# Kernel tuning notes

Measured on AMD Instinct MI355X. Metric: run time of the kernel, lower is better.

## Reference

```python
import jax, jax.numpy as jnp
import numpy as np

EMB, HEAD = 2048, 128

def setup_inputs() -> dict:
    key = jax.random.key(0)
    ks = jax.random.split(key, 7)
    x = jax.random.normal(ks[0], (4, 4096, EMB), dtype=jnp.float32)
    s = 1.0 / np.sqrt(EMB)
    wK = jax.random.normal(ks[1], (EMB, HEAD), dtype=jnp.float32) * s
    bK = jax.random.normal(ks[2], (HEAD,), dtype=jnp.float32) * 0.01
    wQ = jax.random.normal(ks[3], (EMB, HEAD), dtype=jnp.float32) * s
    bQ = jax.random.normal(ks[4], (HEAD,), dtype=jnp.float32) * 0.01
    wV = jax.random.normal(ks[5], (EMB, HEAD), dtype=jnp.float32) * s
    bV = jax.random.normal(ks[6], (HEAD,), dtype=jnp.float32) * 0.01
    return {"x": x, "wK": wK, "bK": bK, "wQ": wQ, "bQ": bQ, "wV": wV, "bV": bV}

def reference(x, wK, bK, wQ, bQ, wV, bV):
    B, S, E = x.shape
    K = x @ wK + bK                      # [B,S,H]
    Q = x @ wQ + bQ
    V = x @ wV + bV
    scale = 1.0 / jnp.sqrt(jnp.float32(HEAD))
    att = jnp.einsum('bqh,bkh->bqk', Q, K) * scale   # [B,S,S]
    causal = jnp.tril(jnp.ones((S, S), dtype=bool))
    att = jnp.where(causal, att, -jnp.inf)
    att = jax.nn.softmax(att, axis=-1)
    return jnp.einsum('bqk,bkh->bqh', att, V)        # [B,S,H]
```

## Files before the change

### kernel.cpp

```cpp
#include <hip/hip_runtime.h>
#include <hip/hip_bf16.h>
#include <math.h>

#define SEQ  4096
#define BATCH 4
#define EMBD 2048
#define HDIM 128

#define SCALE_LOG2E 0.12753102721944556f

typedef __bf16 bf16x8 __attribute__((ext_vector_type(8)));
typedef __bf16 bf16x4 __attribute__((ext_vector_type(4)));
typedef float  f32x4  __attribute__((ext_vector_type(4)));

__device__ __forceinline__ bf16x8 ldfrag(const __bf16* p) {
    return *(const bf16x8*)p;
}

__device__ __forceinline__ void gl_lds16(const __bf16* g, __bf16* l) {
    __builtin_amdgcn_global_load_lds(
        (const __attribute__((address_space(1))) void*)g,
        (__attribute__((address_space(3))) void*)l, 16, 0, 0);
}

__global__ __launch_bounds__(256)
void cvt_x(const float* __restrict__ x, __bf16* __restrict__ xb) {
    size_t idx = (size_t)(blockIdx.x * 256 + threadIdx.x) * 8;
    float4 v0 = *(const float4*)(x + idx);
    float4 v1 = *(const float4*)(x + idx + 4);
    bf16x8 o = { (__bf16)v0.x, (__bf16)v0.y, (__bf16)v0.z, (__bf16)v0.w,
                 (__bf16)v1.x, (__bf16)v1.y, (__bf16)v1.z, (__bf16)v1.w };
    *(bf16x8*)(xb + idx) = o;
}

__global__ __launch_bounds__(256)
void cvt_w(const float* __restrict__ wQ, const float* __restrict__ wK,
           const float* __restrict__ wV, __bf16* __restrict__ wt) {
    const float* w = (blockIdx.z == 0) ? wQ : (blockIdx.z == 1) ? wK : wV;
    __bf16* dst = wt + (size_t)blockIdx.z * HDIM * EMBD;
    int k0 = blockIdx.x * 32;
    int n0 = blockIdx.y * 32;
    __shared__ float t[32][33];
    {
        int r  = threadIdx.x >> 3;
        int c4 = (threadIdx.x & 7) * 4;
        float4 v = *(const float4*)(w + (size_t)(k0 + r) * HDIM + n0 + c4);
        t[r][c4 + 0] = v.x; t[r][c4 + 1] = v.y;
        t[r][c4 + 2] = v.z; t[r][c4 + 3] = v.w;
    }
    __syncthreads();
    {
        int n  = threadIdx.x >> 3;
        int k4 = (threadIdx.x & 7) * 4;
        bf16x4 o = { (__bf16)t[k4 + 0][n], (__bf16)t[k4 + 1][n],
                     (__bf16)t[k4 + 2][n], (__bf16)t[k4 + 3][n] };
        *(bf16x4*)(dst + (size_t)(n0 + n) * EMBD + k0 + k4) = o;
    }
}

__global__ __launch_bounds__(256, 3)
void proj(const __bf16* __restrict__ xb,
          const __bf16* __restrict__ wt,
          __bf16* __restrict__ pout) {
    const int mat  = blockIdx.y;
    const int z    = blockIdx.z;
    const int m0   = blockIdx.x * 128;
    const int kb   = z * (EMBD / 2);
    const int wv   = threadIdx.x >> 6;
    const int lane = threadIdx.x & 63;
    const int ln   = lane & 15;
    const int quad = lane >> 4;
    const int r8   = lane >> 3;
    const int c8   = lane & 7;

    __shared__ __bf16 lA[128 * 64];
    __shared__ __bf16 lB[128 * 64];

    const __bf16* wtm = wt + (size_t)mat * (HDIM * EMBD);
    const __bf16* gaS = xb  + (size_t)(m0 + wv * 32 + r8) * EMBD + kb + (c8 ^ r8) * 8;
    const __bf16* gbS = wtm + (size_t)(wv * 32 + r8) * EMBD + kb + (c8 ^ r8) * 8;
    __bf16* laD = lA + (wv * 32) * 64;
    __bf16* lbD = lB + (wv * 32) * 64;

    const int wm0 = (wv >> 1) * 64;
    const int wn0 = (wv & 1) * 64;

    const f32x4 fzero = {0.f, 0.f, 0.f, 0.f};
    f32x4 acc[4][4];
#pragma unroll
    for (int i = 0; i < 4; i++)
#pragma unroll
        for (int j = 0; j < 4; j++) acc[i][j] = fzero;

    for (int k0 = 0; k0 < EMBD / 2; k0 += 64) {
#pragma unroll
        for (int i = 0; i < 4; i++) {
            gl_lds16(gaS + (size_t)i * 8 * EMBD + k0, laD + i * 8 * 64);
            gl_lds16(gbS + (size_t)i * 8 * EMBD + k0, lbD + i * 8 * 64);
        }
        __syncthreads();
#pragma unroll
        for (int kk = 0; kk < 2; kk++) {
            bf16x8 a[4], bb[4];
#pragma unroll
            for (int i = 0; i < 4; i++)
                a[i] = ldfrag(lA + (wm0 + i * 16 + ln) * 64 +
                              (((quad + 4 * kk) ^ (ln & 7)) * 8));
#pragma unroll
            for (int j = 0; j < 4; j++)
                bb[j] = ldfrag(lB + (wn0 + j * 16 + ln) * 64 +
                               (((quad + 4 * kk) ^ (ln & 7)) * 8));
#pragma unroll
            for (int i = 0; i < 4; i++)
#pragma unroll
                for (int j = 0; j < 4; j++)
                    acc[i][j] = __builtin_amdgcn_mfma_f32_16x16x32_bf16(
                        a[i], bb[j], acc[i][j], 0, 0, 0);
        }
        __syncthreads();
    }

    __bf16* pp = pout + (size_t)(mat * 2 + z) * 16384 * 128;
#pragma unroll
    for (int j = 0; j < 4; j++) {
        int col = wn0 + j * 16 + ln;
#pragma unroll
        for (int i = 0; i < 4; i++) {
            int rowb = m0 + wm0 + i * 16 + quad * 4;
#pragma unroll
            for (int r = 0; r < 4; r++)
                pp[(size_t)(rowb + r) * 128 + col] = (__bf16)acc[i][j][r];
        }
    }
}

__global__ __launch_bounds__(256)
void qkv_fin(const __bf16* __restrict__ pout,
             const float* __restrict__ bQ, const float* __restrict__ bK,
             const float* __restrict__ bV,
             __bf16* __restrict__ qws, __bf16* __restrict__ kws,
             __bf16* __restrict__ vtws) {
    const int mat = blockIdx.y;
    const int r0  = blockIdx.x * 16;
    const int t   = threadIdx.x;
    const int rl  = t >> 4;
    const int cc  = (t & 15) * 8;
    const float* bias = (mat == 0) ? bQ : (mat == 1) ? bK : bV;

    bf16x8 p0 = *(const bf16x8*)(pout +
        ((size_t)(mat * 2 + 0) * 16384 + r0 + rl) * 128 + cc);
    bf16x8 p1 = *(const bf16x8*)(pout +
        ((size_t)(mat * 2 + 1) * 16384 + r0 + rl) * 128 + cc);
    float s[8];
#pragma unroll
    for (int i = 0; i < 8; i++)
        s[i] = (float)p0[i] + (float)p1[i] + bias[cc + i];

    if (mat < 2) {
        __bf16* dst = (mat == 0) ? qws : kws;
        bf16x8 o;
#pragma unroll
        for (int i = 0; i < 8; i++) o[i] = (__bf16)s[i];
        *(bf16x8*)(dst + (size_t)(r0 + rl) * 128 + cc) = o;
    } else {
        __shared__ float sm[16][132];
#pragma unroll
        for (int i = 0; i < 8; i++) sm[rl][cc + i] = s[i];
        __syncthreads();
        int col = t >> 1, sg = (t & 1) * 8;
        int bb = r0 >> 12, s0 = r0 & (SEQ - 1);
        bf16x8 o;
#pragma unroll
        for (int i = 0; i < 8; i++) o[i] = (__bf16)sm[sg + i][col];
        *(bf16x8*)(vtws + ((size_t)bb * HDIM + col) * SEQ + s0 + sg) = o;
    }
}

__global__ __launch_bounds__(256, 2)
void attn(const __bf16* __restrict__ qws, const __bf16* __restrict__ kws,
          const __bf16* __restrict__ vtws,
          float* __restrict__ Opart, float* __restrict__ Lpart) {
    const int blk = blockIdx.x;
    const int b   = (blk & 7) >> 1;
    int wi = ((blk >> 3) << 1) | (blk & 1);
    wi = 287 - wi;
    int a = (int)((sqrtf((float)wi + 1.0f) - 1.0f) * 0.5f);
    while (4 * (a + 1) * (a + 2) <= wi) a++;
    while (a > 0 && 4 * a * (a + 1) > wi) a--;
    const int rem = wi - 4 * a * (a + 1);
    const int qt  = a * 8 + rem / (a + 1);
    const int c   = rem - (rem / (a + 1)) * (a + 1);
    const int q0  = qt * 64;
    const int kt0 = c * 8;
    const int kt1 = (kt0 + 8 < qt + 1) ? (kt0 + 8) : (qt + 1);
    const int slot = b * 288 + wi;

    const int wv   = threadIdx.x >> 6;
    const int lane = threadIdx.x & 63;
    const int ln   = lane & 15;
    const int quad = lane >> 4;

    __shared__ __bf16 lK[2][64 * 128];
    __shared__ __bf16 lV[2][128 * 64];
    __shared__ __bf16 lP[4][16 * 72];

    const __bf16* kws_b = kws + (size_t)b * SEQ * HDIM;
    const __bf16* vt_b  = vtws + (size_t)b * HDIM * SEQ;

    const __bf16* qbase =
        qws + ((size_t)(b * SEQ) + q0 + wv * 16 + ln) * HDIM + quad * 8;
    bf16x8 qf[4];
#pragma unroll
    for (int kk = 0; kk < 4; kk++) qf[kk] = ldfrag(qbase + kk * 32);

    const f32x4 fzero = {0.f, 0.f, 0.f, 0.f};
    float lrun[4];
    f32x4 oacc[8];
#pragma unroll
    for (int r = 0; r < 4; r++) lrun[r] = 0.f;
#pragma unroll
    for (int j = 0; j < 8; j++) oacc[j] = fzero;

    const int krow_i = lane >> 4, kslot = lane & 15;
    const int vrow_i = lane >> 3, vslot = lane & 7;

    auto stageK = [&](int k0, int buf) {
#pragma unroll
        for (int i = 0; i < 4; i++) {
            int row = wv * 16 + i * 4 + krow_i;
            const __bf16* src = kws_b + (size_t)(k0 + row) * HDIM +
                                ((kslot ^ (row & 7)) * 8);
            gl_lds16(src, &lK[buf][(wv * 16 + i * 4) * 128]);
        }
    };
    auto stageV = [&](int k0, int buf) {
#pragma unroll
        for (int i = 0; i < 4; i++) {
            int row = wv * 32 + i * 8 + vrow_i;
            const __bf16* src = vt_b + (size_t)row * SEQ + k0 +
                                ((vslot ^ (row & 7)) * 8);
            gl_lds16(src, &lV[buf][(wv * 32 + i * 8) * 64]);
        }
    };

    stageK(kt0 * 64, 0);
    stageV(kt0 * 64, 0);

    for (int kt = kt0; kt < kt1; kt++) {
        __syncthreads();
        const int cur = (kt - kt0) & 1;
        if (kt + 1 < kt1) {
            stageK((kt + 1) * 64, cur ^ 1);
            stageV((kt + 1) * 64, cur ^ 1);
        }

        f32x4 sacc[4];
#pragma unroll
        for (int j = 0; j < 4; j++) sacc[j] = fzero;
        const __bf16* Kb = lK[cur];
#pragma unroll
        for (int j = 0; j < 4; j++) {
#pragma unroll
            for (int kk = 0; kk < 4; kk++) {
                bf16x8 kf = ldfrag(Kb + (j * 16 + ln) * 128 +
                                   (((quad + 4 * kk) ^ (ln & 7)) * 8));
                sacc[j] = __builtin_amdgcn_mfma_f32_16x16x32_bf16(
                    qf[kk], kf, sacc[j], 0, 0, 0);
            }
        }

        const bool diag = (kt == qt);
#pragma unroll
        for (int j = 0; j < 4; j++) {
#pragma unroll
            for (int r = 0; r < 4; r++) {
                float p = exp2f(sacc[j][r] * SCALE_LOG2E);
                if (diag) {
                    int col = kt * 64 + j * 16 + ln;
                    int row = q0 + wv * 16 + quad * 4 + r;
                    if (col > row) p = 0.f;
                }
                lrun[r] += p;
                lP[wv][(quad * 4 + r) * 72 + j * 16 + ln] = (__bf16)p;
            }
        }

        __builtin_amdgcn_s_waitcnt(0xc07f);
        bf16x8 af0 = ldfrag(&lP[wv][ln * 72 + quad * 8]);
        bf16x8 af1 = ldfrag(&lP[wv][ln * 72 + 32 + quad * 8]);

        const __bf16* Vb = lV[cur];
#pragma unroll
        for (int j = 0; j < 8; j++) {
            bf16x8 v0 = ldfrag(Vb + (j * 16 + ln) * 64 +
                               ((quad ^ (ln & 7)) * 8));
            bf16x8 v1 = ldfrag(Vb + (j * 16 + ln) * 64 +
                               (((quad + 4) ^ (ln & 7)) * 8));
            oacc[j] = __builtin_amdgcn_mfma_f32_16x16x32_bf16(
                af0, v0, oacc[j], 0, 0, 0);
            oacc[j] = __builtin_amdgcn_mfma_f32_16x16x32_bf16(
                af1, v1, oacc[j], 0, 0, 0);
        }
    }

#pragma unroll
    for (int r = 0; r < 4; r++) {
#pragma unroll
        for (int off = 8; off >= 1; off >>= 1)
            lrun[r] += __shfl_xor(lrun[r], off);
    }
    if (ln == 0) {
#pragma unroll
        for (int r = 0; r < 4; r++)
            Lpart[(size_t)slot * 64 + wv * 16 + quad * 4 + r] = lrun[r];
    }
    float* Ob = Opart + (size_t)slot * 8192;
#pragma unroll
    for (int r = 0; r < 4; r++) {
        int row = wv * 16 + quad * 4 + r;
#pragma unroll
        for (int j = 0; j < 8; j++)
            Ob[(size_t)row * 128 + j * 16 + ln] = oacc[j][r];
    }
}

__global__ __launch_bounds__(256)
void attn_fin(const float* __restrict__ Opart, const float* __restrict__ Lpart,
              float* __restrict__ out) {
    const int b  = blockIdx.x >> 6;
    const int qt = blockIdx.x & 63;
    const int a  = qt >> 3;
    const int nch = a + 1;
    const int base = b * 288 + 4 * a * (a + 1) + (qt & 7) * (a + 1);
    const int row = threadIdx.x >> 2;
    const int c0  = (threadIdx.x & 3) * 32;

    float l = 0.f;
    f32x4 o[8];
#pragma unroll
    for (int i = 0; i < 8; i++) o[i] = {0.f, 0.f, 0.f, 0.f};
    for (int ch = 0; ch < nch; ch++) {
        const f32x4* Op = (const f32x4*)(Opart + (size_t)(base + ch) * 8192 +
                                         (size_t)row * 128 + c0);
        l += Lpart[(size_t)(base + ch) * 64 + row];
#pragma unroll
        for (int i = 0; i < 8; i++) o[i] += Op[i];
    }
    float inv = 1.f / l;
    f32x4* orow = (f32x4*)(out + ((size_t)(b * SEQ) + qt * 64 + row) * HDIM + c0);
#pragma unroll
    for (int i = 0; i < 8; i++) orow[i] = o[i] * inv;
}

extern "C" void kernel_launch(void* const* d_in, const int* in_sizes, int n_in,
                              void* d_out, int out_size, void* d_ws,
                              size_t ws_size, hipStream_t stream) {
    const float* x  = (const float*)d_in[0];
    const float* wK = (const float*)d_in[1];
    const float* bK = (const float*)d_in[2];
    const float* wQ = (const float*)d_in[3];
    const float* bQ = (const float*)d_in[4];
    const float* wV = (const float*)d_in[5];
    const float* bV = (const float*)d_in[6];
    float* out = (float*)d_out;

    __bf16* xb   = (__bf16*)d_ws;
    __bf16* wt   = xb + (size_t)BATCH * SEQ * EMBD;
    __bf16* qws  = wt + (size_t)3 * HDIM * EMBD;
    __bf16* kws  = qws + (size_t)BATCH * SEQ * HDIM;
    __bf16* vtws = kws + (size_t)BATCH * SEQ * HDIM;
    __bf16* pout = vtws + (size_t)BATCH * SEQ * HDIM;
    float* Opart = (float*)d_ws;
    float* Lpart = Opart + (size_t)1152 * 8192;

    hipLaunchKernelGGL(cvt_w, dim3(EMBD / 32, HDIM / 32, 3), dim3(256), 0,
                       stream, wQ, wK, wV, wt);
    hipLaunchKernelGGL(cvt_x, dim3((size_t)BATCH * SEQ * EMBD / (8 * 256)),
                       dim3(256), 0, stream, x, xb);
    hipLaunchKernelGGL(proj, dim3(SEQ * BATCH / 128, 3, 2), dim3(256), 0,
                       stream, xb, wt, pout);
    hipLaunchKernelGGL(qkv_fin, dim3(SEQ * BATCH / 16, 3), dim3(256), 0,
                       stream, pout, bQ, bK, bV, qws, kws, vtws);
    hipLaunchKernelGGL(attn, dim3(1152), dim3(256), 0, stream,
                       qws, kws, vtws, Opart, Lpart);
    hipLaunchKernelGGL(attn_fin, dim3(256), dim3(256), 0, stream,
                       Opart, Lpart, out);
}
```

Baseline: 312.3 us.

## Fuse QKV projection with bias epilogue, drop split-K and finalize kernel

The projection kernel now computes all three Q/K/V outputs at once for a 64-row tile using 512 threads. It runs over the full K dimension with double-buffered LDS staging, then adds bias and writes Q, K and the transposed V directly through an LDS staging buffer. This removes the split-K partial buffer, its round trip through global memory, and the separate qkv_fin launch. In exchange it uses about 112KB of LDS per block and launches only 256 blocks, which may leave occupancy and load balance weaker than before.

```diff
diff --git a/kernel.cpp b/kernel.cpp
--- a/kernel.cpp
+++ b/kernel.cpp
@@ -58,121 +58,117 @@
     }
 }
 
-__global__ __launch_bounds__(256, 3)
+__global__ __launch_bounds__(512, 2)
 void proj(const __bf16* __restrict__ xb,
           const __bf16* __restrict__ wt,
-          __bf16* __restrict__ pout) {
-    const int mat  = blockIdx.y;
-    const int z    = blockIdx.z;
-    const int m0   = blockIdx.x * 128;
-    const int kb   = z * (EMBD / 2);
-    const int wv   = threadIdx.x >> 6;
+          const float* __restrict__ bQ, const float* __restrict__ bK,
+          const float* __restrict__ bV,
+          __bf16* __restrict__ qws, __bf16* __restrict__ kws,
+          __bf16* __restrict__ vtws) {
+    const int m0   = blockIdx.x * 64;
+    const int w    = threadIdx.x >> 6;
     const int lane = threadIdx.x & 63;
     const int ln   = lane & 15;
     const int quad = lane >> 4;
-    const int r8   = lane >> 3;
-    const int c8   = lane & 7;
-
-    __shared__ __bf16 lA[128 * 64];
-    __shared__ __bf16 lB[128 * 64];
-
-    const __bf16* wtm = wt + (size_t)mat * (HDIM * EMBD);
-    const __bf16* gaS = xb  + (size_t)(m0 + wv * 32 + r8) * EMBD + kb + (c8 ^ r8) * 8;
-    const __bf16* gbS = wtm + (size_t)(wv * 32 + r8) * EMBD + kb + (c8 ^ r8) * 8;
-    __bf16* laD = lA + (wv * 32) * 64;
-    __bf16* lbD = lB + (wv * 32) * 64;
-
-    const int wm0 = (wv >> 1) * 64;
-    const int wn0 = (wv & 1) * 64;
+    const int lr   = lane >> 3;
+    const int lc   = lane & 7;
+
+    __shared__ __bf16 smem[57344];
+
+    const __bf16* gA = xb + (size_t)(m0 + w * 8 + lr) * EMBD + (lc ^ lr) * 8;
+    const __bf16* gB = wt + (size_t)(w * 48 + lr) * EMBD + (lc ^ lr) * 8;
 
     const f32x4 fzero = {0.f, 0.f, 0.f, 0.f};
-    f32x4 acc[4][4];
+    f32x4 acc[4][3];
 #pragma unroll
     for (int i = 0; i < 4; i++)
 #pragma unroll
-        for (int j = 0; j < 4; j++) acc[i][j] = fzero;
-
-    for (int k0 = 0; k0 < EMBD / 2; k0 += 64) {
-#pragma unroll
-        for (int i = 0; i < 4; i++) {
-            gl_lds16(gaS + (size_t)i * 8 * EMBD + k0, laD + i * 8 * 64);
-            gl_lds16(gbS + (size_t)i * 8 * EMBD + k0, lbD + i * 8 * 64);
-        }
-        __syncthreads();
+        for (int j = 0; j < 3; j++) acc[i][j] = fzero;
+
+    auto stage = [&](int buf, int k0) {
+        __bf16* lA = smem + buf * 28672;
+        __bf16* lB = lA + 4096;
+        gl_lds16(gA + k0, lA + (w * 8) * 64);
+#pragma unroll
+        for (int i = 0; i < 6; i++)
+            gl_lds16(gB + (size_t)(i * 8) * EMBD + k0,
+                     lB + (w * 48 + i * 8) * 64);
+    };
+
+    auto compute = [&](int buf) {
+        const __bf16* lA = smem + buf * 28672;
+        const __bf16* lB = lA + 4096;
 #pragma unroll
         for (int kk = 0; kk < 2; kk++) {
-            bf16x8 a[4], bb[4];
+            bf16x8 a[4], bb[3];
 #pragma unroll
             for (int i = 0; i < 4; i++)
-                a[i] = ldfrag(lA + (wm0 + i * 16 + ln) * 64 +
+                a[i] = ldfrag(lA + (i * 16 + ln) * 64 +
                               (((quad + 4 * kk) ^ (ln & 7)) * 8));
 #pragma unroll
-            for (int j = 0; j < 4; j++)
-                bb[j] = ldfrag(lB + (wn0 + j * 16 + ln) * 64 +
+            for (int j = 0; j < 3; j++)
+                bb[j] = ldfrag(lB + (w * 48 + j * 16 + ln) * 64 +
                                (((quad + 4 * kk) ^ (ln & 7)) * 8));
 #pragma unroll
             for (int i = 0; i < 4; i++)
 #pragma unroll
-                for (int j = 0; j < 4; j++)
+                for (int j = 0; j < 3; j++)
                     acc[i][j] = __builtin_amdgcn_mfma_f32_16x16x32_bf16(
                         a[i], bb[j], acc[i][j], 0, 0, 0);
         }
+    };
+
+    stage(0, 0);
+    __syncthreads();
+    for (int t = 0; t < 32; t++) {
+        const int cur = t & 1;
+        if (t < 31) stage(cur ^ 1, (t + 1) * 64);
+        compute(cur);
         __syncthreads();
     }
 
-    __bf16* pp = pout + (size_t)(mat * 2 + z) * 16384 * 128;
-#pragma unroll
-    for (int j = 0; j < 4; j++) {
-        int col = wn0 + j * 16 + ln;
-#pragma unroll
-        for (int i = 0; i < 4; i++) {
-            int rowb = m0 + wm0 + i * 16 + quad * 4;
+    __bf16* so = smem;
+    constexpr int SOS = 392;
+#pragma unroll
+    for (int j = 0; j < 3; j++) {
+        int c = w * 48 + j * 16 + ln;
+        const float* bp = (c < 128) ? bQ : (c < 256) ? bK : bV;
+        float bv = bp[c & 127];
+#pragma unroll
+        for (int i = 0; i < 4; i++)
 #pragma unroll
             for (int r = 0; r < 4; r++)
-                pp[(size_t)(rowb + r) * 128 + col] = (__bf16)acc[i][j][r];
-        }
-    }
-}
-
-__global__ __launch_bounds__(256)
-void qkv_fin(const __bf16* __restrict__ pout,
-             const float* __restrict__ bQ, const float* __restrict__ bK,
-             const float* __restrict__ bV,
-             __bf16* __restrict__ qws, __bf16* __restrict__ kws,
-             __bf16* __restrict__ vtws) {
-    const int mat = blockIdx.y;
-    const int r0  = blockIdx.x * 16;
-    const int t   = threadIdx.x;
-    const int rl  = t >> 4;
-    const int cc  = (t & 15) * 8;
-    const float* bias = (mat == 0) ? bQ : (mat == 1) ? bK : bV;
-
-    bf16x8 p0 = *(const bf16x8*)(pout +
-        ((size_t)(mat * 2 + 0) * 16384 + r0 + rl) * 128 + cc);
-    bf16x8 p1 = *(const bf16x8*)(pout +
-        ((size_t)(mat * 2 + 1) * 16384 + r0 + rl) * 128 + cc);
-    float s[8];
-#pragma unroll
-    for (int i = 0; i < 8; i++)
-        s[i] = (float)p0[i] + (float)p1[i] + bias[cc + i];
-
-    if (mat < 2) {
-        __bf16* dst = (mat == 0) ? qws : kws;
-        bf16x8 o;
-#pragma unroll
-        for (int i = 0; i < 8; i++) o[i] = (__bf16)s[i];
-        *(bf16x8*)(dst + (size_t)(r0 + rl) * 128 + cc) = o;
-    } else {
-        __shared__ float sm[16][132];
-#pragma unroll
-        for (int i = 0; i < 8; i++) sm[rl][cc + i] = s[i];
-        __syncthreads();
-        int col = t >> 1, sg = (t & 1) * 8;
-        int bb = r0 >> 12, s0 = r0 & (SEQ - 1);
-        bf16x8 o;
-#pragma unroll
-        for (int i = 0; i < 8; i++) o[i] = (__bf16)sm[sg + i][col];
-        *(bf16x8*)(vtws + ((size_t)bb * HDIM + col) * SEQ + s0 + sg) = o;
+                so[(i * 16 + quad * 4 + r) * SOS + c] =
+                    (__bf16)(acc[i][j][r] + bv);
+    }
+    __syncthreads();
+
+    {
+        int row = threadIdx.x >> 3;
+        int c0  = (threadIdx.x & 7) * 32;
+        __bf16* dst = (c0 < 128)
+            ? qws + (size_t)(m0 + row) * HDIM + c0
+            : kws + (size_t)(m0 + row) * HDIM + (c0 - 128);
+#pragma unroll
+        for (int k = 0; k < 4; k++)
+            *(bf16x8*)(dst + k * 8) =
+                *(const bf16x8*)(so + row * SOS + c0 + k * 8);
+    }
+    {
+        int h   = threadIdx.x >> 2;
+        int sc  = (threadIdx.x & 3) * 16;
+        int bb2 = m0 >> 12;
+        int s0g = m0 & (SEQ - 1);
+        bf16x8 o0, o1;
+#pragma unroll
+        for (int ss = 0; ss < 8; ss++)
+            o0[ss] = so[(sc + ss) * SOS + 256 + h];
+#pragma unroll
+        for (int ss = 0; ss < 8; ss++)
+            o1[ss] = so[(sc + 8 + ss) * SOS + 256 + h];
+        __bf16* dst = vtws + ((size_t)bb2 * HDIM + h) * SEQ + s0g + sc;
+        *(bf16x8*)dst = o0;
+        *(bf16x8*)(dst + 8) = o1;
     }
 }
 
@@ -369,7 +365,6 @@
     __bf16* qws  = wt + (size_t)3 * HDIM * EMBD;
     __bf16* kws  = qws + (size_t)BATCH * SEQ * HDIM;
     __bf16* vtws = kws + (size_t)BATCH * SEQ * HDIM;
-    __bf16* pout = vtws + (size_t)BATCH * SEQ * HDIM;
     float* Opart = (float*)d_ws;
     float* Lpart = Opart + (size_t)1152 * 8192;
 
@@ -377,10 +372,8 @@
                        stream, wQ, wK, wV, wt);
     hipLaunchKernelGGL(cvt_x, dim3((size_t)BATCH * SEQ * EMBD / (8 * 256)),
                        dim3(256), 0, stream, x, xb);
-    hipLaunchKernelGGL(proj, dim3(SEQ * BATCH / 128, 3, 2), dim3(256), 0,
-                       stream, xb, wt, pout);
-    hipLaunchKernelGGL(qkv_fin, dim3(SEQ * BATCH / 16, 3), dim3(256), 0,
-                       stream, pout, bQ, bK, bV, qws, kws, vtws);
+    hipLaunchKernelGGL(proj, dim3(SEQ * BATCH / 64), dim3(512), 0, stream,
+                       xb, wt, bQ, bK, bV, qws, kws, vtws);
     hipLaunchKernelGGL(attn, dim3(1152), dim3(256), 0, stream,
                        qws, kws, vtws, Opart, Lpart);
     hipLaunchKernelGGL(attn_fin, dim3(256), dim3(256), 0, stream,
```

Measured after the change: 307.6 us. About the same (-1.5%).
